# Optimization experiments

Hardware: AMD Instinct MI355X
Metric: run time of the kernel (lower is better)

The kernel has to match this reference:

```python
import math
import jax, jax.numpy as jnp
import numpy as np

FACIL_RATE = 2.0
FIRE_THRESH = 0.85
MAX_GATE = 8.0
EPS = 1e-12  # F.normalize eps

B, T, D = 8, 4096, 2048


def _gelu(x):
    # tanh-approx GELU, exactly as in the torch module
    c = math.sqrt(2.0 / math.pi)
    return 0.5 * x * (1.0 + jnp.tanh(c * (x + 0.044715 * x * x * x)))


def _l2norm(v, axis=-1):
    n = jnp.sqrt(jnp.sum(v * v, axis=axis, keepdims=True))
    return v / jnp.maximum(n, EPS)


def setup_inputs() -> dict:
    key = jax.random.key(0)
    k1, k2 = jax.random.split(key)
    x = jax.random.normal(k1, (B, T, D), dtype=jnp.float32)
    pos_buf = jax.random.normal(k2, (T, D), dtype=jnp.float32)
    pos_facil = jnp.ones((T,), dtype=jnp.float32)
    log_k_pos = jnp.asarray(math.log(0.5), dtype=jnp.float32)
    return {"x": x, "log_k_pos": log_k_pos, "pos_buf": pos_buf, "pos_facil": pos_facil}


def reference(x, log_k_pos, pos_buf, pos_facil):
    # steady-state (pass1 complete) path of GELU275.forward
    k_pos = jnp.clip(jnp.exp(log_k_pos), 0.01, 5.0)
    y = _gelu(x)                                   # [B,T,D]
    # everything below the gelu except the final gate multiply runs under
    # no_grad / on y.detach() in torch -> stop_gradient here
    y_det = jax.lax.stop_gradient(y)
    pos_buf_n = _l2norm(jax.lax.stop_gradient(pos_buf))          # [T,D]
    y_n = _l2norm(y_det)                                          # [B,T,D]
    sim = jnp.einsum("btd,td->bt", y_n, pos_buf_n)               # cosine sim [B,T]
    fire_mask = jnp.mean(sim, axis=0) > FIRE_THRESH              # [T]
    pf = jax.lax.stop_gradient(pos_facil)
    facil_t = jnp.where(fire_mask, jnp.minimum(pf * FACIL_RATE, 16.0), pf)  # [T]
    gate = jnp.minimum(1.0 + k_pos * (facil_t[None, :] - 1.0) * sim, MAX_GATE)  # [B,T]
    return y * gate[:, :, None]
```

## Files before the change

kernel.cpp:

```cpp
#include <hip/hip_runtime.h>
#include <math.h>

#define BB 8
#define TT 4096
#define DD 2048
#define THREADS 512
#define NT 8
#define NBLK (TT / NT)

typedef float v4f __attribute__((ext_vector_type(4)));

__device__ __forceinline__ float gelu_fast(float x) {
    const float c1 = 1.5957691216057308f;
    const float c2 = 0.07135481282556483f;
    float e = __expf(-x * fmaf(c2, x * x, c1));
    return x * __builtin_amdgcn_rcpf(1.0f + e);
}

__device__ __forceinline__ void do_step(
    const float* __restrict__ x, const float* __restrict__ pos_buf,
    const float* __restrict__ pos_facil, float* __restrict__ out,
    int t, int par, bool last, int lane, int wave, float kp,
    v4f (&CUR)[8], v4f (&NXT)[8], v4f (&P)[8],
    float (&s_red)[2][17])
{
    const int base = lane * 4;

    if (!last) {
        const float* xr = x + ((size_t)wave * TT + (t + 1)) * DD + base;
#pragma unroll
        for (int c = 0; c < 8; ++c) NXT[c] = *(const v4f*)(xr + c * 256);
    }

    float dot = 0.f, yn2 = 0.f, pn2 = 0.f;
#pragma unroll
    for (int c = 0; c < 8; ++c) {
        v4f v = CUR[c];
        v.x = gelu_fast(v.x); v.y = gelu_fast(v.y);
        v.z = gelu_fast(v.z); v.w = gelu_fast(v.w);
        CUR[c] = v;
        const v4f p = P[c];
        dot += v.x * p.x + v.y * p.y + v.z * p.z + v.w * p.w;
        yn2 += v.x * v.x + v.y * v.y + v.z * v.z + v.w * v.w;
        pn2 += p.x * p.x + p.y * p.y + p.z * p.z + p.w * p.w;
    }

    if (!last) {
        const float* pr = pos_buf + (size_t)(t + 1) * DD + base;
#pragma unroll
        for (int c = 0; c < 8; ++c) P[c] = *(const v4f*)(pr + c * 256);
    }

#pragma unroll
    for (int off = 32; off; off >>= 1) {
        dot += __shfl_xor(dot, off);
        yn2 += __shfl_xor(yn2, off);
        pn2 += __shfl_xor(pn2, off);
    }
    if (lane == 0) {
        s_red[par][wave]      = dot;
        s_red[par][BB + wave] = yn2;
        if (wave == 0) s_red[par][16] = pn2;
    }
    asm volatile("s_waitcnt lgkmcnt(0)" ::: "memory");
    __builtin_amdgcn_s_barrier();
    asm volatile("" ::: "memory");

    const float pnn = fmaxf(sqrtf(s_red[par][16]), 1e-12f);
    float simsum = 0.f, simw = 0.f;
#pragma unroll
    for (int b = 0; b < BB; ++b) {
        const float s = s_red[par][b] *
            __builtin_amdgcn_rcpf(fmaxf(sqrtf(s_red[par][BB + b]), 1e-12f) * pnn);
        simsum += s;
        if (b == wave) simw = s;
    }
    const bool  fire  = (simsum * 0.125f) > 0.85f;
    const float pf    = pos_facil[t];
    const float facil = fire ? fminf(pf * 2.0f, 16.0f) : pf;
    const float g     = fminf(1.0f + kp * (facil - 1.0f) * simw, 8.0f);

    float* orow = out + ((size_t)wave * TT + t) * DD + base;
#pragma unroll
    for (int c = 0; c < 8; ++c) {
        v4f o = CUR[c];
        o.x *= g; o.y *= g; o.z *= g; o.w *= g;
        *(v4f*)(orow + c * 256) = o;
    }
}

__global__ __launch_bounds__(THREADS, 4) void gelu275_fused(
    const float* __restrict__ x,
    const float* __restrict__ log_k_pos,
    const float* __restrict__ pos_buf,
    const float* __restrict__ pos_facil,
    float* __restrict__ out)
{
    const int tid  = threadIdx.x;
    const int lane = tid & 63;
    const int wave = tid >> 6;
    const int t0   = blockIdx.x * NT;

    __shared__ float s_red[2][17];

    const float kp  = fminf(fmaxf(__expf(log_k_pos[0]), 0.01f), 5.0f);
    const int  base = lane * 4;

    v4f A[8], B[8], P[8];

    {
        const float* xr = x + ((size_t)wave * TT + t0) * DD + base;
#pragma unroll
        for (int c = 0; c < 8; ++c) A[c] = *(const v4f*)(xr + c * 256);
        const float* pr = pos_buf + (size_t)t0 * DD + base;
#pragma unroll
        for (int c = 0; c < 8; ++c) P[c] = *(const v4f*)(pr + c * 256);
    }

#pragma unroll
    for (int i = 0; i < NT; i += 2) {
        do_step(x, pos_buf, pos_facil, out, t0 + i,     0, false,
                lane, wave, kp, A, B, P, s_red);
        do_step(x, pos_buf, pos_facil, out, t0 + i + 1, 1, (i + 2 >= NT),
                lane, wave, kp, B, A, P, s_red);
    }
}

extern "C" void kernel_launch(void* const* d_in, const int* in_sizes, int n_in,
                              void* d_out, int out_size, void* d_ws, size_t ws_size,
                              hipStream_t stream) {
    const float* x          = (const float*)d_in[0];
    const float* log_k_pos  = (const float*)d_in[1];
    const float* pos_buf    = (const float*)d_in[2];
    const float* pos_facil  = (const float*)d_in[3];
    float* out              = (float*)d_out;

    dim3 grid(NBLK);
    dim3 block(THREADS);
    gelu275_fused<<<grid, block, 0, stream>>>(x, log_k_pos, pos_buf, pos_facil, out);
}
```

Baseline: 124.2 us.

## Split fused GELU gate kernel into separate sim, gate, and apply kernels

```diff
diff --git a/kernel.cpp b/kernel.cpp
--- a/kernel.cpp
+++ b/kernel.cpp
@@ -4,9 +4,6 @@
 #define BB 8
 #define TT 4096
 #define DD 2048
-#define THREADS 512
-#define NT 8
-#define NBLK (TT / NT)
 
 typedef float v4f __attribute__((ext_vector_type(4)));
 
@@ -17,40 +14,36 @@
     return x * __builtin_amdgcn_rcpf(1.0f + e);
 }
 
-__device__ __forceinline__ void do_step(
-    const float* __restrict__ x, const float* __restrict__ pos_buf,
-    const float* __restrict__ pos_facil, float* __restrict__ out,
-    int t, int par, bool last, int lane, int wave, float kp,
-    v4f (&CUR)[8], v4f (&NXT)[8], v4f (&P)[8],
-    float (&s_red)[2][17])
+__global__ __launch_bounds__(256) void k_sims(
+    const float* __restrict__ x,
+    const float* __restrict__ pos_buf,
+    float* __restrict__ sims)
 {
-    const int base = lane * 4;
+    const int pair = blockIdx.x * 4 + (threadIdx.x >> 6);
+    const int lane = threadIdx.x & 63;
+    const int t    = pair >> 3;
+    const int b    = pair & 7;
 
-    if (!last) {
-        const float* xr = x + ((size_t)wave * TT + (t + 1)) * DD + base;
+    const float* xr = x       + ((size_t)b * TT + t) * DD + lane * 4;
+    const float* pr = pos_buf + (size_t)t * DD + lane * 4;
+
+    v4f xv[8], pv[8];
 #pragma unroll
-        for (int c = 0; c < 8; ++c) NXT[c] = *(const v4f*)(xr + c * 256);
-    }
+    for (int c = 0; c < 8; ++c) xv[c] = *(const v4f*)(xr + c * 256);
+#pragma unroll
+    for (int c = 0; c < 8; ++c) pv[c] = *(const v4f*)(pr + c * 256);
 
     float dot = 0.f, yn2 = 0.f, pn2 = 0.f;
 #pragma unroll
     for (int c = 0; c < 8; ++c) {
-        v4f v = CUR[c];
+        v4f v = xv[c];
         v.x = gelu_fast(v.x); v.y = gelu_fast(v.y);
         v.z = gelu_fast(v.z); v.w = gelu_fast(v.w);
-        CUR[c] = v;
-        const v4f p = P[c];
+        const v4f p = pv[c];
         dot += v.x * p.x + v.y * p.y + v.z * p.z + v.w * p.w;
         yn2 += v.x * v.x + v.y * v.y + v.z * v.z + v.w * v.w;
         pn2 += p.x * p.x + p.y * p.y + p.z * p.z + p.w * p.w;
     }
-
-    if (!last) {
-        const float* pr = pos_buf + (size_t)(t + 1) * DD + base;
-#pragma unroll
-        for (int c = 0; c < 8; ++c) P[c] = *(const v4f*)(pr + c * 256);
-    }
-
 #pragma unroll
     for (int off = 32; off; off >>= 1) {
         dot += __shfl_xor(dot, off);
@@ -58,71 +51,61 @@
         pn2 += __shfl_xor(pn2, off);
     }
     if (lane == 0) {
-        s_red[par][wave]      = dot;
-        s_red[par][BB + wave] = yn2;
-        if (wave == 0) s_red[par][16] = pn2;
+        const float yn = fmaxf(sqrtf(yn2), 1e-12f);
+        const float pn = fmaxf(sqrtf(pn2), 1e-12f);
+        sims[pair] = dot / (yn * pn);
     }
-    asm volatile("s_waitcnt lgkmcnt(0)" ::: "memory");
-    __builtin_amdgcn_s_barrier();
-    asm volatile("" ::: "memory");
+}
 
-    const float pnn = fmaxf(sqrtf(s_red[par][16]), 1e-12f);
-    float simsum = 0.f, simw = 0.f;
+__global__ __launch_bounds__(256) void k_gates(
+    const float* __restrict__ sims,
+    const float* __restrict__ pos_facil,
+    const float* __restrict__ log_k_pos,
+    float* __restrict__ gates)
+{
+    const int t = blockIdx.x * 256 + threadIdx.x;
+    const float kp = fminf(fmaxf(__expf(log_k_pos[0]), 0.01f), 5.0f);
+
+    float s[BB];
+    float simsum = 0.f;
 #pragma unroll
     for (int b = 0; b < BB; ++b) {
-        const float s = s_red[par][b] *
-            __builtin_amdgcn_rcpf(fmaxf(sqrtf(s_red[par][BB + b]), 1e-12f) * pnn);
-        simsum += s;
-        if (b == wave) simw = s;
+        s[b] = sims[t * 8 + b];
+        simsum += s[b];
     }
     const bool  fire  = (simsum * 0.125f) > 0.85f;
     const float pf    = pos_facil[t];
     const float facil = fire ? fminf(pf * 2.0f, 16.0f) : pf;
-    const float g     = fminf(1.0f + kp * (facil - 1.0f) * simw, 8.0f);
+#pragma unroll
+    for (int b = 0; b < BB; ++b)
+        gates[t * 8 + b] = fminf(1.0f + kp * (facil - 1.0f) * s[b], 8.0f);
+}
 
-    float* orow = out + ((size_t)wave * TT + t) * DD + base;
+__global__ __launch_bounds__(512) void k_apply(
+    const float* __restrict__ x,
+    const float* __restrict__ gates,
+    float* __restrict__ out)
+{
+    const int t    = blockIdx.x;
+    const int lane = threadIdx.x & 63;
+    const int b    = threadIdx.x >> 6;
+
+    const float g = gates[t * 8 + b];
+
+    const float* xr = x   + ((size_t)b * TT + t) * DD + lane * 4;
+    float*       po = out + ((size_t)b * TT + t) * DD + lane * 4;
+
+    v4f xv[8];
+#pragma unroll
+    for (int c = 0; c < 8; ++c) xv[c] = *(const v4f*)(xr + c * 256);
 #pragma unroll
     for (int c = 0; c < 8; ++c) {
-        v4f o = CUR[c];
-        o.x *= g; o.y *= g; o.z *= g; o.w *= g;
-        *(v4f*)(orow + c * 256) = o;
-    }
-}
-
-__global__ __launch_bounds__(THREADS, 4) void gelu275_fused(
-    const float* __restrict__ x,
-    const float* __restrict__ log_k_pos,
-    const float* __restrict__ pos_buf,
-    const float* __restrict__ pos_facil,
-    float* __restrict__ out)
-{
-    const int tid  = threadIdx.x;
-    const int lane = tid & 63;
-    const int wave = tid >> 6;
-    const int t0   = blockIdx.x * NT;
-
-    __shared__ float s_red[2][17];
-
-    const float kp  = fminf(fmaxf(__expf(log_k_pos[0]), 0.01f), 5.0f);
-    const int  base = lane * 4;
-
-    v4f A[8], B[8], P[8];
-
-    {
-        const float* xr = x + ((size_t)wave * TT + t0) * DD + base;
-#pragma unroll
-        for (int c = 0; c < 8; ++c) A[c] = *(const v4f*)(xr + c * 256);
-        const float* pr = pos_buf + (size_t)t0 * DD + base;
-#pragma unroll
-        for (int c = 0; c < 8; ++c) P[c] = *(const v4f*)(pr + c * 256);
-    }
-
-#pragma unroll
-    for (int i = 0; i < NT; i += 2) {
-        do_step(x, pos_buf, pos_facil, out, t0 + i,     0, false,
-                lane, wave, kp, A, B, P, s_red);
-        do_step(x, pos_buf, pos_facil, out, t0 + i + 1, 1, (i + 2 >= NT),
-                lane, wave, kp, B, A, P, s_red);
+        v4f o = xv[c];
+        o.x = gelu_fast(o.x) * g;
+        o.y = gelu_fast(o.y) * g;
+        o.z = gelu_fast(o.z) * g;
+        o.w = gelu_fast(o.w) * g;
+        *(v4f*)(po + c * 256) = o;
     }
 }
 
@@ -135,7 +118,11 @@
     const float* pos_facil  = (const float*)d_in[3];
     float* out              = (float*)d_out;
 
-    dim3 grid(NBLK);
-    dim3 block(THREADS);
-    gelu275_fused<<<grid, block, 0, stream>>>(x, log_k_pos, pos_buf, pos_facil, out);
+    float* sims  = (float*)d_ws;
+    float* gates = sims + (size_t)TT * BB;
+
+    k_sims <<<dim3((TT * BB) / 4), dim3(256), 0, stream>>>(x, pos_buf, sims);
+    k_gates<<<dim3(TT / 256),      dim3(256), 0, stream>>>(sims, pos_facil,
+                                                           log_k_pos, gates);
+    k_apply<<<dim3(TT),            dim3(512), 0, stream>>>(x, gates, out);
 }
```

Result: slower. 189.8 us (+52.8%).

## Drop pos_buf register prefetch, halve rows per block, raise occupancy bound

Applied to the files above, without the earlier changes.

```diff
diff --git a/kernel.cpp b/kernel.cpp
--- a/kernel.cpp
+++ b/kernel.cpp
@@ -5,7 +5,7 @@
 #define TT 4096
 #define DD 2048
 #define THREADS 512
-#define NT 8
+#define NT 4
 #define NBLK (TT / NT)
 
 typedef float v4f __attribute__((ext_vector_type(4)));
@@ -18,37 +18,30 @@
 }
 
 __device__ __forceinline__ void do_step(
-    const float* __restrict__ x, const float* __restrict__ pos_buf,
-    const float* __restrict__ pos_facil, float* __restrict__ out,
+    const float* __restrict__ xp,
+    const float* __restrict__ pp,
+    const float* __restrict__ pos_facil, float* __restrict__ op,
     int t, int par, bool last, int lane, int wave, float kp,
-    v4f (&CUR)[8], v4f (&NXT)[8], v4f (&P)[8],
+    v4f (&CUR)[8], v4f (&NXT)[8],
     float (&s_red)[2][17])
 {
-    const int base = lane * 4;
-
     if (!last) {
-        const float* xr = x + ((size_t)wave * TT + (t + 1)) * DD + base;
 #pragma unroll
-        for (int c = 0; c < 8; ++c) NXT[c] = *(const v4f*)(xr + c * 256);
+        for (int c = 0; c < 8; ++c)
+            NXT[c] = *(const v4f*)(xp + DD + c * 256);
     }
 
     float dot = 0.f, yn2 = 0.f, pn2 = 0.f;
 #pragma unroll
     for (int c = 0; c < 8; ++c) {
+        const v4f p = *(const v4f*)(pp + c * 256);
         v4f v = CUR[c];
         v.x = gelu_fast(v.x); v.y = gelu_fast(v.y);
         v.z = gelu_fast(v.z); v.w = gelu_fast(v.w);
         CUR[c] = v;
-        const v4f p = P[c];
         dot += v.x * p.x + v.y * p.y + v.z * p.z + v.w * p.w;
         yn2 += v.x * v.x + v.y * v.y + v.z * v.z + v.w * v.w;
         pn2 += p.x * p.x + p.y * p.y + p.z * p.z + p.w * p.w;
-    }
-
-    if (!last) {
-        const float* pr = pos_buf + (size_t)(t + 1) * DD + base;
-#pragma unroll
-        for (int c = 0; c < 8; ++c) P[c] = *(const v4f*)(pr + c * 256);
     }
 
 #pragma unroll
@@ -80,16 +73,15 @@
     const float facil = fire ? fminf(pf * 2.0f, 16.0f) : pf;
     const float g     = fminf(1.0f + kp * (facil - 1.0f) * simw, 8.0f);
 
-    float* orow = out + ((size_t)wave * TT + t) * DD + base;
 #pragma unroll
     for (int c = 0; c < 8; ++c) {
         v4f o = CUR[c];
         o.x *= g; o.y *= g; o.z *= g; o.w *= g;
-        *(v4f*)(orow + c * 256) = o;
+        *(v4f*)(op + c * 256) = o;
     }
 }
 
-__global__ __launch_bounds__(THREADS, 4) void gelu275_fused(
+__global__ __launch_bounds__(THREADS, 6) void gelu275_fused(
     const float* __restrict__ x,
     const float* __restrict__ log_k_pos,
     const float* __restrict__ pos_buf,
@@ -103,26 +95,26 @@
 
     __shared__ float s_red[2][17];
 
-    const float kp  = fminf(fmaxf(__expf(log_k_pos[0]), 0.01f), 5.0f);
-    const int  base = lane * 4;
+    const float kp   = fminf(fmaxf(__expf(log_k_pos[0]), 0.01f), 5.0f);
+    const int   base = lane * 4;
 
-    v4f A[8], B[8], P[8];
+    const float* xp = x       + ((size_t)wave * TT + t0) * DD + base;
+    const float* pp = pos_buf + (size_t)t0 * DD + base;
+    float*       op = out     + ((size_t)wave * TT + t0) * DD + base;
 
-    {
-        const float* xr = x + ((size_t)wave * TT + t0) * DD + base;
+    v4f A[8], B[8];
+
 #pragma unroll
-        for (int c = 0; c < 8; ++c) A[c] = *(const v4f*)(xr + c * 256);
-        const float* pr = pos_buf + (size_t)t0 * DD + base;
-#pragma unroll
-        for (int c = 0; c < 8; ++c) P[c] = *(const v4f*)(pr + c * 256);
-    }
+    for (int c = 0; c < 8; ++c) A[c] = *(const v4f*)(xp + c * 256);
 
 #pragma unroll
     for (int i = 0; i < NT; i += 2) {
-        do_step(x, pos_buf, pos_facil, out, t0 + i,     0, false,
-                lane, wave, kp, A, B, P, s_red);
-        do_step(x, pos_buf, pos_facil, out, t0 + i + 1, 1, (i + 2 >= NT),
-                lane, wave, kp, B, A, P, s_red);
+        do_step(xp, pp, pos_facil, op, t0 + i, 0, false,
+                lane, wave, kp, A, B, s_red);
+        xp += DD; pp += DD; op += DD;
+        do_step(xp, pp, pos_facil, op, t0 + i + 1, 1, (i + 2 >= NT),
+                lane, wave, kp, B, A, s_red);
+        xp += DD; pp += DD; op += DD;
     }
 }
 
```

Result: slower. 143.7 us (+15.7%).

## Stage x and pos_buf rows through LDS with async global-to-LDS double buffering

Applied to the files above, without the earlier changes.

```diff
diff --git a/kernel.cpp b/kernel.cpp
--- a/kernel.cpp
+++ b/kernel.cpp
@@ -7,6 +7,7 @@
 #define THREADS 512
 #define NT 8
 #define NBLK (TT / NT)
+#define SMEM_BYTES ((2 * (BB * DD + DD)) * 4)
 
 typedef float v4f __attribute__((ext_vector_type(4)));
 
@@ -17,112 +18,118 @@
     return x * __builtin_amdgcn_rcpf(1.0f + e);
 }
 
-__device__ __forceinline__ void do_step(
-    const float* __restrict__ x, const float* __restrict__ pos_buf,
-    const float* __restrict__ pos_facil, float* __restrict__ out,
-    int t, int par, bool last, int lane, int wave, float kp,
-    v4f (&CUR)[8], v4f (&NXT)[8], v4f (&P)[8],
-    float (&s_red)[2][17])
-{
-    const int base = lane * 4;
-
-    if (!last) {
-        const float* xr = x + ((size_t)wave * TT + (t + 1)) * DD + base;
-#pragma unroll
-        for (int c = 0; c < 8; ++c) NXT[c] = *(const v4f*)(xr + c * 256);
-    }
-
-    float dot = 0.f, yn2 = 0.f, pn2 = 0.f;
-#pragma unroll
-    for (int c = 0; c < 8; ++c) {
-        v4f v = CUR[c];
-        v.x = gelu_fast(v.x); v.y = gelu_fast(v.y);
-        v.z = gelu_fast(v.z); v.w = gelu_fast(v.w);
-        CUR[c] = v;
-        const v4f p = P[c];
-        dot += v.x * p.x + v.y * p.y + v.z * p.z + v.w * p.w;
-        yn2 += v.x * v.x + v.y * v.y + v.z * v.z + v.w * v.w;
-        pn2 += p.x * p.x + p.y * p.y + p.z * p.z + p.w * p.w;
-    }
-
-    if (!last) {
-        const float* pr = pos_buf + (size_t)(t + 1) * DD + base;
-#pragma unroll
-        for (int c = 0; c < 8; ++c) P[c] = *(const v4f*)(pr + c * 256);
-    }
-
-#pragma unroll
-    for (int off = 32; off; off >>= 1) {
-        dot += __shfl_xor(dot, off);
-        yn2 += __shfl_xor(yn2, off);
-        pn2 += __shfl_xor(pn2, off);
-    }
-    if (lane == 0) {
-        s_red[par][wave]      = dot;
-        s_red[par][BB + wave] = yn2;
-        if (wave == 0) s_red[par][16] = pn2;
-    }
-    asm volatile("s_waitcnt lgkmcnt(0)" ::: "memory");
-    __builtin_amdgcn_s_barrier();
-    asm volatile("" ::: "memory");
-
-    const float pnn = fmaxf(sqrtf(s_red[par][16]), 1e-12f);
-    float simsum = 0.f, simw = 0.f;
-#pragma unroll
-    for (int b = 0; b < BB; ++b) {
-        const float s = s_red[par][b] *
-            __builtin_amdgcn_rcpf(fmaxf(sqrtf(s_red[par][BB + b]), 1e-12f) * pnn);
-        simsum += s;
-        if (b == wave) simw = s;
-    }
-    const bool  fire  = (simsum * 0.125f) > 0.85f;
-    const float pf    = pos_facil[t];
-    const float facil = fire ? fminf(pf * 2.0f, 16.0f) : pf;
-    const float g     = fminf(1.0f + kp * (facil - 1.0f) * simw, 8.0f);
-
-    float* orow = out + ((size_t)wave * TT + t) * DD + base;
-#pragma unroll
-    for (int c = 0; c < 8; ++c) {
-        v4f o = CUR[c];
-        o.x *= g; o.y *= g; o.z *= g; o.w *= g;
-        *(v4f*)(orow + c * 256) = o;
-    }
+__device__ __forceinline__ void gl2lds(const float* g, float* l) {
+    __builtin_amdgcn_global_load_lds(
+        (const __attribute__((address_space(1))) void*)g,
+        (__attribute__((address_space(3))) void*)l, 16, 0, 0);
 }
 
-__global__ __launch_bounds__(THREADS, 4) void gelu275_fused(
+__global__ __launch_bounds__(THREADS, 2) void gelu275_fused(
     const float* __restrict__ x,
     const float* __restrict__ log_k_pos,
     const float* __restrict__ pos_buf,
     const float* __restrict__ pos_facil,
     float* __restrict__ out)
 {
+    extern __shared__ __align__(16) float smem[];
+    float* const xbuf0 = smem;
+    float* const xbuf1 = smem + BB * DD;
+    float* const pbuf0 = smem + 2 * BB * DD;
+    float* const pbuf1 = pbuf0 + DD;
+    __shared__ float s_red[2][17];
+
     const int tid  = threadIdx.x;
     const int lane = tid & 63;
     const int wave = tid >> 6;
     const int t0   = blockIdx.x * NT;
+    const int base = lane * 4;
 
-    __shared__ float s_red[2][17];
-
-    const float kp  = fminf(fmaxf(__expf(log_k_pos[0]), 0.01f), 5.0f);
-    const int  base = lane * 4;
-
-    v4f A[8], B[8], P[8];
+    const float kp = fminf(fmaxf(__expf(log_k_pos[0]), 0.01f), 5.0f);
+    float pfv[NT];
+#pragma unroll
+    for (int i = 0; i < NT; ++i) pfv[i] = pos_facil[t0 + i];
 
     {
-        const float* xr = x + ((size_t)wave * TT + t0) * DD + base;
+        const float* xrow = x + ((size_t)wave * TT + t0) * DD;
 #pragma unroll
-        for (int c = 0; c < 8; ++c) A[c] = *(const v4f*)(xr + c * 256);
-        const float* pr = pos_buf + (size_t)t0 * DD + base;
-#pragma unroll
-        for (int c = 0; c < 8; ++c) P[c] = *(const v4f*)(pr + c * 256);
+        for (int c = 0; c < 8; ++c)
+            gl2lds(xrow + c * 256 + base, xbuf0 + wave * DD + c * 256);
+        gl2lds(pos_buf + (size_t)t0 * DD + wave * 256 + base,
+               pbuf0 + wave * 256);
     }
 
 #pragma unroll
-    for (int i = 0; i < NT; i += 2) {
-        do_step(x, pos_buf, pos_facil, out, t0 + i,     0, false,
-                lane, wave, kp, A, B, P, s_red);
-        do_step(x, pos_buf, pos_facil, out, t0 + i + 1, 1, (i + 2 >= NT),
-                lane, wave, kp, B, A, P, s_red);
+    for (int i = 0; i < NT; ++i) {
+        float* const xb = (i & 1) ? xbuf1 : xbuf0;
+        float* const pb = (i & 1) ? pbuf1 : pbuf0;
+
+        if (i == 0) { asm volatile("s_waitcnt vmcnt(0)" ::: "memory"); }
+        else        { asm volatile("s_waitcnt vmcnt(8)" ::: "memory"); }
+        __builtin_amdgcn_s_barrier();
+        asm volatile("" ::: "memory");
+
+        if (i + 1 < NT) {
+            float* const xn = (i & 1) ? xbuf0 : xbuf1;
+            float* const pn = (i & 1) ? pbuf0 : pbuf1;
+            const float* xrow = x + ((size_t)wave * TT + (t0 + i + 1)) * DD;
+#pragma unroll
+            for (int c = 0; c < 8; ++c)
+                gl2lds(xrow + c * 256 + base, xn + wave * DD + c * 256);
+            gl2lds(pos_buf + (size_t)(t0 + i + 1) * DD + wave * 256 + base,
+                   pn + wave * 256);
+        }
+
+        v4f Y[8];
+        float dot = 0.f, yn2 = 0.f, pn2 = 0.f;
+#pragma unroll
+        for (int c = 0; c < 8; ++c) {
+            v4f v       = *(const v4f*)(xb + wave * DD + c * 256 + base);
+            const v4f p = *(const v4f*)(pb + c * 256 + base);
+            v.x = gelu_fast(v.x); v.y = gelu_fast(v.y);
+            v.z = gelu_fast(v.z); v.w = gelu_fast(v.w);
+            Y[c] = v;
+            dot += v.x * p.x + v.y * p.y + v.z * p.z + v.w * p.w;
+            yn2 += v.x * v.x + v.y * v.y + v.z * v.z + v.w * v.w;
+            pn2 += p.x * p.x + p.y * p.y + p.z * p.z + p.w * p.w;
+        }
+
+#pragma unroll
+        for (int off = 32; off; off >>= 1) {
+            dot += __shfl_xor(dot, off);
+            yn2 += __shfl_xor(yn2, off);
+            pn2 += __shfl_xor(pn2, off);
+        }
+        if (lane == 0) {
+            s_red[i & 1][wave]     = dot;
+            s_red[i & 1][8 + wave] = yn2;
+            if (wave == 0) s_red[i & 1][16] = pn2;
+        }
+        asm volatile("s_waitcnt lgkmcnt(0)" ::: "memory");
+        __builtin_amdgcn_s_barrier();
+        asm volatile("" ::: "memory");
+
+        const float pnn = fmaxf(sqrtf(s_red[i & 1][16]), 1e-12f);
+        float simsum = 0.f, simw = 0.f;
+#pragma unroll
+        for (int bb = 0; bb < BB; ++bb) {
+            const float s = s_red[i & 1][bb] *
+                __builtin_amdgcn_rcpf(
+                    fmaxf(sqrtf(s_red[i & 1][8 + bb]), 1e-12f) * pnn);
+            simsum += s;
+            if (bb == wave) simw = s;
+        }
+        const bool  fire  = (simsum * 0.125f) > 0.85f;
+        const float pf    = pfv[i];
+        const float facil = fire ? fminf(pf * 2.0f, 16.0f) : pf;
+        const float g     = fminf(1.0f + kp * (facil - 1.0f) * simw, 8.0f);
+
+        float* orow = out + ((size_t)wave * TT + (t0 + i)) * DD + base;
+#pragma unroll
+        for (int c = 0; c < 8; ++c) {
+            v4f o = Y[c];
+            o.x *= g; o.y *= g; o.z *= g; o.w *= g;
+            *(v4f*)(orow + c * 256) = o;
+        }
     }
 }
 
@@ -135,7 +142,12 @@
     const float* pos_facil  = (const float*)d_in[3];
     float* out              = (float*)d_out;
 
+    (void)hipFuncSetAttribute((const void*)gelu275_fused,
+                              hipFuncAttributeMaxDynamicSharedMemorySize,
+                              SMEM_BYTES);
+
     dim3 grid(NBLK);
     dim3 block(THREADS);
-    gelu275_fused<<<grid, block, 0, stream>>>(x, log_k_pos, pos_buf, pos_facil, out);
+    gelu275_fused<<<grid, block, SMEM_BYTES, stream>>>(
+        x, log_k_pos, pos_buf, pos_facil, out);
 }
```

Result: faster. 120.7 us (-2.8%).
